# Kernel tuning notes

Hardware: AMD Instinct MI355X
Metric: run time of the kernel (lower is better)

Reference implementation:

```python
import jax, jax.numpy as jnp
import numpy as np

NV, T, CIN, CV, P, NB, H, W, G, SL = 50000, 16, 8, 64, 8, 120000, 512, 512, 16, 4
EPS = 1e-5


def mish(x):
    return x * jnp.tanh(jax.nn.softplus(x))


def bn(x, gamma, beta, axes):
    # BatchNorm in training mode: biased batch stats over `axes`.
    m = x.mean(axes, keepdims=True)
    v = x.var(axes, keepdims=True)
    return (x - m) * jax.lax.rsqrt(v + EPS) * gamma + beta


def fe3(x, Wt, g, b):
    # FELayer on 3D input [N, L, Cin]: Linear -> BN over channel -> Mish
    y = jnp.einsum('nlc,oc->nlo', x, Wt)
    return mish(bn(y, g, b, (0, 1)))


def vfe(x, Wt, g, b):
    # VFELayer: FELayer -> max over points -> broadcast-concat
    p = fe3(x, Wt, g, b)  # [N, T, C/2]
    a = p.max(axis=1, keepdims=True)
    return jnp.concatenate([p, jnp.broadcast_to(a, p.shape)], axis=2)


def setup_inputs() -> dict:
    key = jax.random.key(0)
    ks = jax.random.split(key, 32)
    wn = lambda k, s: jax.random.normal(k, s, jnp.float32) * 0.1
    gm = lambda k, s: 1.0 + jax.random.normal(k, s, jnp.float32) * 0.1
    bt = lambda k, s: jax.random.normal(k, s, jnp.float32) * 0.1
    inp = {}
    inp['voxels'] = jax.random.normal(ks[0], (NV, T, CIN), jnp.float32)
    inp['voxelmask'] = (jax.random.uniform(ks[1], (NV, T, 1)) > 0.2).astype(jnp.float32)
    inp['bevmask'] = (jax.random.uniform(ks[2], (NB, 1, P)) > 0.2).astype(jnp.float32)
    # params
    inp['W_vfe1'] = wn(ks[3], (8, CIN));   inp['g_vfe1'] = gm(ks[4], (8,));   inp['b_vfe1'] = bt(ks[5], (8,))
    inp['W_vfe2'] = wn(ks[6], (32, 16));   inp['g_vfe2'] = gm(ks[7], (32,));  inp['b_vfe2'] = bt(ks[8], (32,))
    inp['W_vfe3'] = wn(ks[9], (CV, CV));   inp['g_vfe3'] = gm(ks[10], (CV,)); inp['b_vfe3'] = bt(ks[11], (CV,))
    inp['W_vfe4'] = wn(ks[12], (CV, CV));  inp['g_vfe4'] = gm(ks[13], (CV,)); inp['b_vfe4'] = bt(ks[14], (CV,))
    inp['W_bfe1'] = wn(ks[15], (G, P, P)); inp['g_bfe1'] = gm(ks[16], (G, P)); inp['b_bfe1'] = bt(ks[17], (G, P))
    inp['W_bfe2'] = wn(ks[18], (G, 2, P)); inp['g_bfe2'] = gm(ks[19], (G, 2)); inp['b_bfe2'] = bt(ks[20], (G, 2))
    inp['W_bfe3'] = wn(ks[21], (128, 128)); inp['g_bfe3'] = gm(ks[22], (128,)); inp['b_bfe3'] = bt(ks[23], (128,))
    # int args
    inp['bevsidx'] = jax.random.randint(ks[24], (NB, P), 0, NV)
    flat = jax.random.permutation(ks[25], H * W)[:NB]  # unique scatter targets
    inp['bevcoors'] = jnp.stack([flat // W, flat % W], axis=1)
    return inp


def reference(voxels, voxelmask, bevmask,
              W_vfe1, g_vfe1, b_vfe1, W_vfe2, g_vfe2, b_vfe2,
              W_vfe3, g_vfe3, b_vfe3, W_vfe4, g_vfe4, b_vfe4,
              W_bfe1, g_bfe1, b_bfe1, W_bfe2, g_bfe2, b_bfe2,
              W_bfe3, g_bfe3, b_bfe3, bevsidx, bevcoors):
    x1 = vfe(voxels, W_vfe1, g_vfe1, b_vfe1)               # [NV, T, 16]
    x2 = vfe(x1, W_vfe2, g_vfe2, b_vfe2) * voxelmask       # [NV, T, 64]
    x3 = fe3(x2, W_vfe3, g_vfe3, b_vfe3)
    x4 = fe3(x3, W_vfe4, g_vfe4, b_vfe4) * voxelmask + x2
    voxelwise = x4.max(axis=1)                             # [NV, 64]

    bevs = voxelwise[bevsidx]                              # [NB, P, 64]
    # x0 = [NB, 64, P] -> 16 groups of 4 channel-slices -> [NB, G, SL, P]
    xg = bevs.transpose(0, 2, 1).reshape(bevs.shape[0], G, SL, P)
    h = jnp.einsum('ngcp,gqp->ngcq', xg, W_bfe1)           # [NB, G, SL, P]
    h = mish(bn(h, g_bfe1[:, None, :], b_bfe1[:, None, :], (0, 2)))
    h = h * bevmask[:, None]                               # [NB,1,1,P] broadcast
    h = jnp.einsum('ngcp,gqp->ngcq', h, W_bfe2)            # [NB, G, SL, 2]
    h = mish(bn(h, g_bfe2[:, None, :], b_bfe2[:, None, :], (0, 2)))
    # torch cat over dim=-1 across groups -> [NB, SL, G, 2] -> [NB, 128]
    x17 = h.transpose(0, 2, 1, 3).reshape(h.shape[0], 128)

    def bfe3(z):
        return mish(bn(z @ W_bfe3.T, g_bfe3, b_bfe3, (0,)))

    x18 = bfe3(x17)
    x19 = bfe3(x18) + x17                                  # NOTE: original reuses bfe3 (bfe4 unused)

    bevmap = jnp.zeros((H, W, 128), voxels.dtype)
    bevmap = bevmap.at[bevcoors[:, 0], bevcoors[:, 1]].set(x19)
    return bevmap.transpose(2, 1, 0)                       # [128, W, H]
```

## Files before the change

kernel.cpp:

```cpp
#include <hip/hip_runtime.h>
#include <math.h>

#define NV_   50000
#define T16_  16
#define NVT_  800000
#define NB_   120000
#define G_    16
#define P_    8
#define H_    512
#define W_    512

#define OF_Y34    0ul
#define OF_Y2     51200000ul
#define OF_Y1     76800000ul
#define OF_VW     83200000ul
#define OF_INV    86400000ul
#define OF_PRE17  0ul
#define OF_X17    16000000ul
#define OF_Y1819  32000000ul
#define STATS_BYTE 346648576ul

#define D_ST1 0
#define D_ST2 16
#define D_ST3 80
#define D_ST4 208
#define D_SB1 336
#define D_SB2 592
#define D_S18 656
#define D_S19 912
#define D_TOTAL 1168

#define LB_HEAVY __launch_bounds__(256, 2)
#define LB_LIGHT __launch_bounds__(256, 4)

__device__ __forceinline__ float mishf(float x) {
  float e = __expf(x);
  float u = 1.0f + e;
  return x - 2.0f * x / (u * u + 1.0f);
}

template <int N>
__device__ __forceinline__ void wave_red_sum(float* v) {
#pragma unroll
  for (int d = 1; d < 64; d <<= 1) {
#pragma unroll
    for (int i = 0; i < N; i++) v[i] += __shfl_xor(v[i], d, 64);
  }
}

__global__ void LB_LIGHT k_inv(const int* __restrict__ coors, int* __restrict__ inv) {
  int n = blockIdx.x * 256 + threadIdx.x;
  if (n < NB_) {
    int h = coors[2 * n], w = coors[2 * n + 1];
    inv[h * W_ + w] = n;
  }
}

__global__ void LB_LIGHT k1(const float* __restrict__ vox, const float* __restrict__ W1,
                   float* __restrict__ y1, double* __restrict__ st) {
  __shared__ float wl[64];
  __shared__ float lst[16];
  int t = threadIdx.x;
  if (t < 64) wl[t] = W1[t];
  if (t < 16) lst[t] = 0.f;
  __syncthreads();
  size_t s = (size_t)blockIdx.x * 256 + t;
  const float4* vp = (const float4*)(vox + s * 8);
  float4 a0 = vp[0], a1 = vp[1];
  float x[8] = {a0.x, a0.y, a0.z, a0.w, a1.x, a1.y, a1.z, a1.w};
  float y[8];
#pragma unroll
  for (int o = 0; o < 8; o++) {
    float a = 0.f;
#pragma unroll
    for (int c = 0; c < 8; c++) a += x[c] * wl[o * 8 + c];
    y[o] = a;
  }
  float4* yp = (float4*)(y1 + s * 8);
  yp[0] = make_float4(y[0], y[1], y[2], y[3]);
  yp[1] = make_float4(y[4], y[5], y[6], y[7]);
  float v[16];
#pragma unroll
  for (int i = 0; i < 8; i++) { v[i] = y[i]; v[8 + i] = y[i] * y[i]; }
  wave_red_sum<16>(v);
  if ((t & 63) == 0) {
#pragma unroll
    for (int i = 0; i < 16; i++) atomicAdd(&lst[i], v[i]);
  }
  __syncthreads();
  if (t < 16) atomicAdd(&st[t], (double)lst[t]);
}

__global__ void LB_HEAVY k2(const float* __restrict__ y1, const double* __restrict__ st1,
                   const float* __restrict__ g1, const float* __restrict__ b1,
                   const float* __restrict__ W2, float* __restrict__ y2,
                   double* __restrict__ st2) {
  __shared__ float wl[512];
  __shared__ float ab[8][2];
  __shared__ float lst[64];
  int t = threadIdx.x;
  wl[t] = W2[t];
  wl[256 + t] = W2[256 + t];
  if (t < 8) {
    double m = st1[t] / (double)NVT_;
    double var = st1[8 + t] / (double)NVT_ - m * m;
    if (var < 0) var = 0;
    float A = (float)((double)g1[t] / sqrt(var + 1e-5));
    ab[t][0] = A; ab[t][1] = b1[t] - (float)m * A;
  }
  if (t < 64) lst[t] = 0.f;
  __syncthreads();
  size_t s = (size_t)blockIdx.x * 256 + t;
  const float4* yp = (const float4*)(y1 + s * 8);
  float4 f0 = yp[0], f1 = yp[1];
  float in[8] = {f0.x, f0.y, f0.z, f0.w, f1.x, f1.y, f1.z, f1.w};
  float xr[16];
#pragma unroll
  for (int c = 0; c < 8; c++) xr[c] = mishf(in[c] * ab[c][0] + ab[c][1]);
#pragma unroll
  for (int c = 0; c < 8; c++) xr[8 + c] = xr[c];
#pragma unroll
  for (int d = 1; d < 16; d <<= 1) {
#pragma unroll
    for (int c = 0; c < 8; c++)
      xr[8 + c] = fmaxf(xr[8 + c], __shfl_xor(xr[8 + c], d, 64));
  }
  float yo[32];
#pragma unroll
  for (int o = 0; o < 32; o++) {
    float a = 0.f;
    const float4* wp = (const float4*)(wl + o * 16);
#pragma unroll
    for (int c4 = 0; c4 < 4; c4++) {
      float4 w4 = wp[c4];
      a += xr[c4 * 4 + 0] * w4.x + xr[c4 * 4 + 1] * w4.y +
           xr[c4 * 4 + 2] * w4.z + xr[c4 * 4 + 3] * w4.w;
    }
    yo[o] = a;
  }
  float4* op = (float4*)(y2 + s * 32);
#pragma unroll
  for (int j = 0; j < 8; j++)
    op[j] = make_float4(yo[j * 4], yo[j * 4 + 1], yo[j * 4 + 2], yo[j * 4 + 3]);
#pragma unroll
  for (int ch = 0; ch < 4; ch++) {
    float v[16];
#pragma unroll
    for (int i = 0; i < 8; i++) {
      v[i] = yo[ch * 8 + i]; v[8 + i] = v[i] * v[i];
    }
    wave_red_sum<16>(v);
    if ((t & 63) == 0) {
#pragma unroll
      for (int i = 0; i < 8; i++) {
        atomicAdd(&lst[ch * 8 + i], v[i]);
        atomicAdd(&lst[32 + ch * 8 + i], v[8 + i]);
      }
    }
  }
  __syncthreads();
  if (t < 64) atomicAdd(&st2[t], (double)lst[t]);
}

__global__ void LB_HEAVY k3(const float* __restrict__ y2, const double* __restrict__ st2,
                   const float* __restrict__ g2, const float* __restrict__ b2,
                   const float* __restrict__ vmask, const float* __restrict__ W3,
                   float* __restrict__ y3, double* __restrict__ st3) {
  __shared__ float ab[32][2];
  __shared__ float lst[128];
  int t = threadIdx.x;
  if (t < 32) {
    double m = st2[t] / (double)NVT_;
    double var = st2[32 + t] / (double)NVT_ - m * m;
    if (var < 0) var = 0;
    float A = (float)((double)g2[t] / sqrt(var + 1e-5));
    ab[t][0] = A; ab[t][1] = b2[t] - (float)m * A;
  }
  if (t < 128) lst[t] = 0.f;
  __syncthreads();
  size_t s = (size_t)blockIdx.x * 256 + t;
  float xr[64];
  const float4* yp = (const float4*)(y2 + s * 32);
#pragma unroll
  for (int j = 0; j < 8; j++) {
    float4 f = yp[j];
    xr[j * 4 + 0] = mishf(f.x * ab[j * 4 + 0][0] + ab[j * 4 + 0][1]);
    xr[j * 4 + 1] = mishf(f.y * ab[j * 4 + 1][0] + ab[j * 4 + 1][1]);
    xr[j * 4 + 2] = mishf(f.z * ab[j * 4 + 2][0] + ab[j * 4 + 2][1]);
    xr[j * 4 + 3] = mishf(f.w * ab[j * 4 + 3][0] + ab[j * 4 + 3][1]);
  }
#pragma unroll
  for (int c = 0; c < 32; c++) xr[32 + c] = xr[c];
#pragma unroll
  for (int d = 1; d < 16; d <<= 1) {
#pragma unroll
    for (int c = 0; c < 32; c++)
      xr[32 + c] = fmaxf(xr[32 + c], __shfl_xor(xr[32 + c], d, 64));
  }
  float m = vmask[s];
#pragma unroll
  for (int c = 0; c < 64; c++) xr[c] *= m;
#pragma unroll
  for (int oc = 0; oc < 4; oc++) {
    float yo[16];
#pragma unroll
    for (int o = 0; o < 16; o++) {
      float a = 0.f;
      const float4* wp = (const float4*)(W3 + (oc * 16 + o) * 64);
#pragma unroll
      for (int c4 = 0; c4 < 16; c4++) {
        float4 w4 = wp[c4];
        a += xr[c4 * 4 + 0] * w4.x + xr[c4 * 4 + 1] * w4.y +
             xr[c4 * 4 + 2] * w4.z + xr[c4 * 4 + 3] * w4.w;
      }
      yo[o] = a;
    }
    float4* op = (float4*)(y3 + s * 64 + oc * 16);
#pragma unroll
    for (int j = 0; j < 4; j++)
      op[j] = make_float4(yo[j * 4], yo[j * 4 + 1], yo[j * 4 + 2], yo[j * 4 + 3]);
    float v[32];
#pragma unroll
    for (int i = 0; i < 16; i++) { v[i] = yo[i]; v[16 + i] = yo[i] * yo[i]; }
    wave_red_sum<32>(v);
    if ((t & 63) == 0) {
#pragma unroll
      for (int i = 0; i < 16; i++) {
        atomicAdd(&lst[oc * 16 + i], v[i]);
        atomicAdd(&lst[64 + oc * 16 + i], v[16 + i]);
      }
    }
  }
  __syncthreads();
  if (t < 128) atomicAdd(&st3[t], (double)lst[t]);
}

__global__ void LB_HEAVY k4(float* y34, const double* __restrict__ st3,
                   const float* __restrict__ g3, const float* __restrict__ b3,
                   const float* __restrict__ W4, double* __restrict__ st4) {
  __shared__ float ab[64][2];
  __shared__ float lst[128];
  int t = threadIdx.x;
  if (t < 64) {
    double m = st3[t] / (double)NVT_;
    double var = st3[64 + t] / (double)NVT_ - m * m;
    if (var < 0) var = 0;
    float A = (float)((double)g3[t] / sqrt(var + 1e-5));
    ab[t][0] = A; ab[t][1] = b3[t] - (float)m * A;
  }
  if (t < 128) lst[t] = 0.f;
  __syncthreads();
  size_t s = (size_t)blockIdx.x * 256 + t;
  float xr[64];
  const float4* yp = (const float4*)(y34 + s * 64);
#pragma unroll
  for (int j = 0; j < 16; j++) {
    float4 f = yp[j];
    xr[j * 4 + 0] = mishf(f.x * ab[j * 4 + 0][0] + ab[j * 4 + 0][1]);
    xr[j * 4 + 1] = mishf(f.y * ab[j * 4 + 1][0] + ab[j * 4 + 1][1]);
    xr[j * 4 + 2] = mishf(f.z * ab[j * 4 + 2][0] + ab[j * 4 + 2][1]);
    xr[j * 4 + 3] = mishf(f.w * ab[j * 4 + 3][0] + ab[j * 4 + 3][1]);
  }
#pragma unroll
  for (int oc = 0; oc < 4; oc++) {
    float yo[16];
#pragma unroll
    for (int o = 0; o < 16; o++) {
      float a = 0.f;
      const float4* wp = (const float4*)(W4 + (oc * 16 + o) * 64);
#pragma unroll
      for (int c4 = 0; c4 < 16; c4++) {
        float4 w4 = wp[c4];
        a += xr[c4 * 4 + 0] * w4.x + xr[c4 * 4 + 1] * w4.y +
             xr[c4 * 4 + 2] * w4.z + xr[c4 * 4 + 3] * w4.w;
      }
      yo[o] = a;
    }
    float4* op = (float4*)(y34 + s * 64 + oc * 16);
#pragma unroll
    for (int j = 0; j < 4; j++)
      op[j] = make_float4(yo[j * 4], yo[j * 4 + 1], yo[j * 4 + 2], yo[j * 4 + 3]);
    float v[32];
#pragma unroll
    for (int i = 0; i < 16; i++) { v[i] = yo[i]; v[16 + i] = yo[i] * yo[i]; }
    wave_red_sum<32>(v);
    if ((t & 63) == 0) {
#pragma unroll
      for (int i = 0; i < 16; i++) {
        atomicAdd(&lst[oc * 16 + i], v[i]);
        atomicAdd(&lst[64 + oc * 16 + i], v[16 + i]);
      }
    }
  }
  __syncthreads();
  if (t < 128) atomicAdd(&st4[t], (double)lst[t]);
}

__global__ void LB_HEAVY k5(const float* __restrict__ y34, const double* __restrict__ st4,
                   const float* __restrict__ g4, const float* __restrict__ b4,
                   const float* __restrict__ y2, const double* __restrict__ st2,
                   const float* __restrict__ g2, const float* __restrict__ b2,
                   const float* __restrict__ vmask, float* __restrict__ vw) {
  __shared__ float ab4[64][2];
  __shared__ float ab2[32][2];
  int t = threadIdx.x;
  if (t < 64) {
    double m = st4[t] / (double)NVT_;
    double var = st4[64 + t] / (double)NVT_ - m * m;
    if (var < 0) var = 0;
    float A = (float)((double)g4[t] / sqrt(var + 1e-5));
    ab4[t][0] = A; ab4[t][1] = b4[t] - (float)m * A;
  } else if (t >= 128 && t < 160) {
    int c = t - 128;
    double m = st2[c] / (double)NVT_;
    double var = st2[32 + c] / (double)NVT_ - m * m;
    if (var < 0) var = 0;
    float A = (float)((double)g2[c] / sqrt(var + 1e-5));
    ab2[c][0] = A; ab2[c][1] = b2[c] - (float)m * A;
  }
  __syncthreads();
  size_t s = (size_t)blockIdx.x * 256 + t;
  int v = (int)(s >> 4), ti = t & 15;
  float msk = vmask[s];
  float xr[64];
  const float4* y2p = (const float4*)(y2 + s * 32);
#pragma unroll
  for (int j = 0; j < 8; j++) {
    float4 f = y2p[j];
    xr[j * 4 + 0] = mishf(f.x * ab2[j * 4 + 0][0] + ab2[j * 4 + 0][1]);
    xr[j * 4 + 1] = mishf(f.y * ab2[j * 4 + 1][0] + ab2[j * 4 + 1][1]);
    xr[j * 4 + 2] = mishf(f.z * ab2[j * 4 + 2][0] + ab2[j * 4 + 2][1]);
    xr[j * 4 + 3] = mishf(f.w * ab2[j * 4 + 3][0] + ab2[j * 4 + 3][1]);
  }
#pragma unroll
  for (int c = 0; c < 32; c++) xr[32 + c] = xr[c];
#pragma unroll
  for (int d = 1; d < 16; d <<= 1) {
#pragma unroll
    for (int c = 0; c < 32; c++)
      xr[32 + c] = fmaxf(xr[32 + c], __shfl_xor(xr[32 + c], d, 64));
  }
#pragma unroll
  for (int c = 0; c < 64; c++) xr[c] *= msk;
  const float4* yp = (const float4*)(y34 + s * 64);
#pragma unroll
  for (int j = 0; j < 16; j++) {
    float4 f = yp[j];
    xr[j * 4 + 0] += mishf(f.x * ab4[j * 4 + 0][0] + ab4[j * 4 + 0][1]) * msk;
    xr[j * 4 + 1] += mishf(f.y * ab4[j * 4 + 1][0] + ab4[j * 4 + 1][1]) * msk;
    xr[j * 4 + 2] += mishf(f.z * ab4[j * 4 + 2][0] + ab4[j * 4 + 2][1]) * msk;
    xr[j * 4 + 3] += mishf(f.w * ab4[j * 4 + 3][0] + ab4[j * 4 + 3][1]) * msk;
  }
#pragma unroll
  for (int d = 1; d < 16; d <<= 1) {
#pragma unroll
    for (int c = 0; c < 64; c++)
      xr[c] = fmaxf(xr[c], __shfl_xor(xr[c], d, 64));
  }
  *(float4*)(vw + (size_t)v * 64 + ti * 4) =
      make_float4(xr[ti * 4], xr[ti * 4 + 1], xr[ti * 4 + 2], xr[ti * 4 + 3]);
}

__global__ void LB_HEAVY k6(const float* __restrict__ vw, const int* __restrict__ idx,
                   const float* __restrict__ Wb1, double* __restrict__ sb1) {
  __shared__ float wl[1024];
  __shared__ float lst[256];
  int t = threadIdx.x;
  for (int i = t; i < 1024; i += 256) {
    int g = i >> 6, qp = i & 63;
    wl[qp * 16 + g] = Wb1[i];
  }
  lst[t] = 0.f;
  __syncthreads();
  int g = t & 15, nl = t >> 4;
  float ss[8] = {0, 0, 0, 0, 0, 0, 0, 0}, sq[8] = {0, 0, 0, 0, 0, 0, 0, 0};
  for (int it = 0; it < 16; ++it) {
    int n = blockIdx.x * 256 + it * 16 + nl;
    if (n < NB_) {
      int id[8];
#pragma unroll
      for (int p = 0; p < 8; p++) id[p] = idx[n * 8 + p];
      float xg[4][8];
#pragma unroll
      for (int p = 0; p < 8; p++) {
        float4 f = *(const float4*)(vw + (size_t)id[p] * 64 + g * 4);
        xg[0][p] = f.x; xg[1][p] = f.y; xg[2][p] = f.z; xg[3][p] = f.w;
      }
#pragma unroll
      for (int q = 0; q < 8; q++) {
        float wq[8];
#pragma unroll
        for (int p = 0; p < 8; p++) wq[p] = wl[(q * 8 + p) * 16 + g];
#pragma unroll
        for (int c = 0; c < 4; c++) {
          float a = 0.f;
#pragma unroll
          for (int p = 0; p < 8; p++) a += xg[c][p] * wq[p];
          ss[q] += a; sq[q] += a * a;
        }
      }
    }
  }
#pragma unroll
  for (int d = 16; d < 64; d <<= 1) {
#pragma unroll
    for (int q = 0; q < 8; q++) {
      ss[q] += __shfl_xor(ss[q], d, 64);
      sq[q] += __shfl_xor(sq[q], d, 64);
    }
  }
  if ((t & 48) == 0) {
#pragma unroll
    for (int q = 0; q < 8; q++) {
      atomicAdd(&lst[g * 8 + q], ss[q]);
      atomicAdd(&lst[128 + g * 8 + q], sq[q]);
    }
  }
  __syncthreads();
  atomicAdd(&sb1[t], (double)lst[t]);
}

__global__ void LB_HEAVY k7(const float* __restrict__ vw, const int* __restrict__ idx,
                   const float* __restrict__ Wb1, const double* __restrict__ sb1,
                   const float* __restrict__ gb1, const float* __restrict__ bb1,
                   const float* __restrict__ bmask, const float* __restrict__ Wb2,
                   float* __restrict__ pre17, double* __restrict__ sb2) {
  __shared__ float wl[1024];
  __shared__ float w2l[256];
  __shared__ float ab[128][2];
  __shared__ float lst[64];
  int t = threadIdx.x;
  for (int i = t; i < 1024; i += 256) {
    int g = i >> 6, qp = i & 63;
    wl[qp * 16 + g] = Wb1[i];
  }
  {
    int g = t >> 4, qq = t & 15;
    w2l[qq * 16 + g] = Wb2[t];
  }
  if (t < 128) {
    double m = sb1[t] / 480000.0;
    double var = sb1[128 + t] / 480000.0 - m * m;
    if (var < 0) var = 0;
    float A = (float)((double)gb1[t] / sqrt(var + 1e-5));
    ab[t][0] = A; ab[t][1] = bb1[t] - (float)m * A;
  }
  if (t < 64) lst[t] = 0.f;
  __syncthreads();
  int g = t & 15, nl = t >> 4;
  float s2[2] = {0, 0}, q2s[2] = {0, 0};
  for (int it = 0; it < 16; ++it) {
    int n = blockIdx.x * 256 + it * 16 + nl;
    if (n < NB_) {
      int id[8];
      float bmv[8];
#pragma unroll
      for (int p = 0; p < 8; p++) { id[p] = idx[n * 8 + p]; bmv[p] = bmask[n * 8 + p]; }
      float xg[4][8];
#pragma unroll
      for (int p = 0; p < 8; p++) {
        float4 f = *(const float4*)(vw + (size_t)id[p] * 64 + g * 4);
        xg[0][p] = f.x; xg[1][p] = f.y; xg[2][p] = f.z; xg[3][p] = f.w;
      }
      float th[4][8];
#pragma unroll
      for (int q = 0; q < 8; q++) {
        float wq[8];
#pragma unroll
        for (int p = 0; p < 8; p++) wq[p] = wl[(q * 8 + p) * 16 + g];
        float A = ab[g * 8 + q][0], B = ab[g * 8 + q][1];
#pragma unroll
        for (int c = 0; c < 4; c++) {
          float a = 0.f;
#pragma unroll
          for (int p = 0; p < 8; p++) a += xg[c][p] * wq[p];
          th[c][q] = mishf(a * A + B) * bmv[q];
        }
      }
#pragma unroll
      for (int c = 0; c < 4; c++) {
        float v0 = 0.f, v1 = 0.f;
#pragma unroll
        for (int q = 0; q < 8; q++) {
          v0 += th[c][q] * w2l[q * 16 + g];
          v1 += th[c][q] * w2l[(8 + q) * 16 + g];
        }
        *(float2*)(pre17 + (size_t)n * 128 + c * 32 + g * 2) = make_float2(v0, v1);
        s2[0] += v0; q2s[0] += v0 * v0;
        s2[1] += v1; q2s[1] += v1 * v1;
      }
    }
  }
#pragma unroll
  for (int d = 16; d < 64; d <<= 1) {
#pragma unroll
    for (int j = 0; j < 2; j++) {
      s2[j] += __shfl_xor(s2[j], d, 64);
      q2s[j] += __shfl_xor(q2s[j], d, 64);
    }
  }
  if ((t & 48) == 0) {
#pragma unroll
    for (int j = 0; j < 2; j++) {
      atomicAdd(&lst[g * 2 + j], s2[j]);
      atomicAdd(&lst[32 + g * 2 + j], q2s[j]);
    }
  }
  __syncthreads();
  if (t < 64) atomicAdd(&sb2[t], (double)lst[t]);
}

template <int MODE>
__global__ void LB_HEAVY kgemm(const float* xin, const double* __restrict__ stin,
                      const float* __restrict__ gam, const float* __restrict__ bet,
                      const float* __restrict__ Wt, float* xact_out,
                      float* yout, double* __restrict__ stout) {
  __shared__ float xs[32 * 129];
  __shared__ float wsh[128 * 33];
  __shared__ float ab[128][2];
  __shared__ float lst[256];
  int t = threadIdx.x;
  const int nch = (MODE == 0) ? 32 : 128;
  const double den = (MODE == 0) ? 480000.0 : 120000.0;
  if (t < nch) {
    double m = stin[t] / den;
    double var = stin[nch + t] / den - m * m;
    if (var < 0) var = 0;
    float A = (float)((double)gam[t] / sqrt(var + 1e-5));
    ab[t][0] = A; ab[t][1] = bet[t] - (float)m * A;
  }
  lst[t] = 0.f;
  __syncthreads();
  int s0 = blockIdx.x * 128;
  int oc = t & 7, sc = t >> 3;
  int cl = t & 31, sl8 = t >> 5;
  float acc[64];
#pragma unroll
  for (int i = 0; i < 64; i++) acc[i] = 0.f;
  for (int cb = 0; cb < 128; cb += 32) {
#pragma unroll
    for (int r = 0; r < 16; r++) {
      int slocal = r * 8 + sl8;
      int sg = s0 + slocal;
      float v = 0.f;
      if (sg < NB_) {
        float h = xin[(size_t)sg * 128 + cb + cl];
        if (MODE == 0) {
          v = mishf(h * ab[cl][0] + ab[cl][1]);
          xact_out[(size_t)sg * 128 + cb + cl] = v;
        } else {
          v = mishf(h * ab[cb + cl][0] + ab[cb + cl][1]);
        }
      }
      xs[cl * 129 + slocal] = v;
    }
#pragma unroll
    for (int r = 0; r < 16; r++) {
      int o = r * 8 + sl8;
      wsh[o * 33 + cl] = Wt[o * 128 + cb + cl];
    }
    __syncthreads();
#pragma unroll 4
    for (int c = 0; c < 32; c++) {
      float xv[4];
#pragma unroll
      for (int i = 0; i < 4; i++) xv[i] = xs[c * 129 + sc * 4 + i];
#pragma unroll
      for (int k = 0; k < 16; k++) {
        float wv = wsh[(k * 8 + oc) * 33 + c];
#pragma unroll
        for (int i = 0; i < 4; i++) acc[k * 4 + i] += wv * xv[i];
      }
    }
    __syncthreads();
  }
  float ssum[16], ssq[16];
#pragma unroll
  for (int k = 0; k < 16; k++) { ssum[k] = 0.f; ssq[k] = 0.f; }
#pragma unroll
  for (int i = 0; i < 4; i++) {
    int sg = s0 + sc * 4 + i;
    if (sg < NB_) {
#pragma unroll
      for (int k = 0; k < 16; k++) {
        float v = acc[k * 4 + i];
        yout[(size_t)sg * 128 + k * 8 + oc] = v;
        ssum[k] += v; ssq[k] += v * v;
      }
    }
  }
#pragma unroll
  for (int d = 8; d < 64; d <<= 1) {
#pragma unroll
    for (int k = 0; k < 16; k++) {
      ssum[k] += __shfl_xor(ssum[k], d, 64);
      ssq[k] += __shfl_xor(ssq[k], d, 64);
    }
  }
  if ((t & 63) < 8) {
#pragma unroll
    for (int k = 0; k < 16; k++) {
      atomicAdd(&lst[k * 8 + oc], ssum[k]);
      atomicAdd(&lst[128 + k * 8 + oc], ssq[k]);
    }
  }
  __syncthreads();
  atomicAdd(&stout[t], (double)lst[t]);
}

__global__ void LB_LIGHT k10(const float* __restrict__ y19, const float* __restrict__ x17,
                    const double* __restrict__ s19, const float* __restrict__ g3,
                    const float* __restrict__ b3, const int* __restrict__ inv,
                    float* __restrict__ out) {
  __shared__ float buf[256 * 32];
  __shared__ float ab[32][2];
  int t = threadIdx.x;
  int w = blockIdx.x, hh = blockIdx.y, ch = blockIdx.z;
  if (t < 32) {
    int c = ch * 32 + t;
    double m = s19[c] / 120000.0;
    double var = s19[128 + c] / 120000.0 - m * m;
    if (var < 0) var = 0;
    float A = (float)((double)g3[c] / sqrt(var + 1e-5));
    ab[t][0] = A; ab[t][1] = b3[c] - (float)m * A;
  }
  __syncthreads();
  int lane = t & 31, rg = t >> 5;
#pragma unroll 4
  for (int r = 0; r < 32; r++) {
    int h_l = r * 8 + rg;
    int h = hh * 256 + h_l;
    int n = inv[h * W_ + w];
    float v = 0.f;
    if (n >= 0) {
      float y = y19[(size_t)n * 128 + ch * 32 + lane];
      v = mishf(y * ab[lane][0] + ab[lane][1]) +
          x17[(size_t)n * 128 + ch * 32 + lane];
    }
    buf[h_l * 32 + (lane ^ (h_l & 31))] = v;
  }
  __syncthreads();
#pragma unroll 4
  for (int c_l = 0; c_l < 32; c_l++) {
    out[(size_t)(ch * 32 + c_l) * (W_ * H_) + (size_t)w * H_ + hh * 256 + t] =
        buf[t * 32 + (c_l ^ (t & 31))];
  }
}

extern "C" void kernel_launch(void* const* d_in, const int* in_sizes, int n_in,
                              void* d_out, int out_size, void* d_ws, size_t ws_size,
                              hipStream_t stream) {
  const float* voxels = (const float*)d_in[0];
  const float* vmask = (const float*)d_in[1];
  const float* bmask = (const float*)d_in[2];
  const float* W1 = (const float*)d_in[3];
  const float* g1 = (const float*)d_in[4];
  const float* b1 = (const float*)d_in[5];
  const float* W2 = (const float*)d_in[6];
  const float* g2 = (const float*)d_in[7];
  const float* b2 = (const float*)d_in[8];
  const float* W3 = (const float*)d_in[9];
  const float* g3 = (const float*)d_in[10];
  const float* b3 = (const float*)d_in[11];
  const float* W4 = (const float*)d_in[12];
  const float* g4 = (const float*)d_in[13];
  const float* b4 = (const float*)d_in[14];
  const float* Wb1 = (const float*)d_in[15];
  const float* gb1 = (const float*)d_in[16];
  const float* bb1 = (const float*)d_in[17];
  const float* Wb2 = (const float*)d_in[18];
  const float* gb2 = (const float*)d_in[19];
  const float* bb2 = (const float*)d_in[20];
  const float* Wb3 = (const float*)d_in[21];
  const float* gb3 = (const float*)d_in[22];
  const float* bb3 = (const float*)d_in[23];
  const int* bevsidx = (const int*)d_in[24];
  const int* bevcoors = (const int*)d_in[25];

  float* ws = (float*)d_ws;
  float* y1 = ws + OF_Y1;
  float* y2 = ws + OF_Y2;
  float* y34 = ws + OF_Y34;
  float* vw = ws + OF_VW;
  float* pre17 = ws + OF_PRE17;
  float* x17 = ws + OF_X17;
  float* y1819 = ws + OF_Y1819;
  int* inv = (int*)(ws + OF_INV);
  double* stats = (double*)((char*)d_ws + STATS_BYTE);

  hipMemsetAsync(stats, 0, D_TOTAL * sizeof(double), stream);
  hipMemsetAsync(inv, 0xFF, (size_t)(H_ * W_) * sizeof(int), stream);

  k_inv<<<469, 256, 0, stream>>>(bevcoors, inv);
  k1<<<3125, 256, 0, stream>>>(voxels, W1, y1, stats + D_ST1);
  k2<<<3125, 256, 0, stream>>>(y1, stats + D_ST1, g1, b1, W2, y2, stats + D_ST2);
  k3<<<3125, 256, 0, stream>>>(y2, stats + D_ST2, g2, b2, vmask, W3, y34,
                               stats + D_ST3);
  k4<<<3125, 256, 0, stream>>>(y34, stats + D_ST3, g3, b3, W4, stats + D_ST4);
  k5<<<3125, 256, 0, stream>>>(y34, stats + D_ST4, g4, b4, y2, stats + D_ST2,
                               g2, b2, vmask, vw);
  k6<<<469, 256, 0, stream>>>(vw, bevsidx, Wb1, stats + D_SB1);
  k7<<<469, 256, 0, stream>>>(vw, bevsidx, Wb1, stats + D_SB1, gb1, bb1, bmask,
                              Wb2, pre17, stats + D_SB2);
  kgemm<0><<<938, 256, 0, stream>>>(pre17, stats + D_SB2, gb2, bb2, Wb3, x17,
                                    y1819, stats + D_S18);
  kgemm<1><<<938, 256, 0, stream>>>(y1819, stats + D_S18, gb3, bb3, Wb3, nullptr,
                                    y1819, stats + D_S19);
  dim3 g10(512, 2, 4);
  k10<<<g10, 256, 0, stream>>>(y1819, x17, stats + D_S19, gb3, bb3, inv,
                               (float*)d_out);
}
```

Measured before the change: 1.707 ms.

## Restructure VFE3/VFE4 GEMMs: weights in registers, rows staged through shared memory

k3 and k4 previously gave each thread one point row. Each thread held 64 activations and re-read all 64x64 weights from global/cache, then did heavy wave shuffles for the stats. Now each thread owns one output channel with its weight row in registers. Blocks loop over 16-row chunks staged in shared memory (mish, max-over-points and mask done cooperatively), and per-channel sums are accumulated in registers so the shuffle reductions go away. This trades register pressure and weight reloads for more barriers per chunk and a fixed 2500x20x16 tiling of the 800000 rows.

```diff
diff --git a/kernel.cpp b/kernel.cpp
--- a/kernel.cpp
+++ b/kernel.cpp
@@ -33,6 +33,9 @@
 #define LB_HEAVY __launch_bounds__(256, 2)
 #define LB_LIGHT __launch_bounds__(256, 4)
 
+#define GEMM_BLOCKS 2500
+#define GEMM_CHUNKS 20
+
 __device__ __forceinline__ float mishf(float x) {
   float e = __expf(x);
   float u = 1.0f + e;
@@ -162,13 +165,19 @@
   if (t < 64) atomicAdd(&st2[t], (double)lst[t]);
 }
 
-__global__ void LB_HEAVY k3(const float* __restrict__ y2, const double* __restrict__ st2,
-                   const float* __restrict__ g2, const float* __restrict__ b2,
-                   const float* __restrict__ vmask, const float* __restrict__ W3,
-                   float* __restrict__ y3, double* __restrict__ st3) {
+__global__ void __launch_bounds__(256, 4)
+k3(const float* __restrict__ y2, const double* __restrict__ st2,
+   const float* __restrict__ g2, const float* __restrict__ b2,
+   const float* __restrict__ vmask, const float* __restrict__ W3,
+   float* __restrict__ y3, double* __restrict__ st3) {
   __shared__ float ab[32][2];
+  __shared__ float x2s[16][32];
+  __shared__ float xmax[32];
+  __shared__ float msk[16];
+  __shared__ float xs[16][64];
   __shared__ float lst[128];
   int t = threadIdx.x;
+  int o = t & 63, wv = t >> 6;
   if (t < 32) {
     double m = st2[t] / (double)NVT_;
     double var = st2[32 + t] / (double)NVT_ - m * m;
@@ -177,70 +186,76 @@
     ab[t][0] = A; ab[t][1] = b2[t] - (float)m * A;
   }
   if (t < 128) lst[t] = 0.f;
-  __syncthreads();
-  size_t s = (size_t)blockIdx.x * 256 + t;
-  float xr[64];
-  const float4* yp = (const float4*)(y2 + s * 32);
-#pragma unroll
-  for (int j = 0; j < 8; j++) {
-    float4 f = yp[j];
-    xr[j * 4 + 0] = mishf(f.x * ab[j * 4 + 0][0] + ab[j * 4 + 0][1]);
-    xr[j * 4 + 1] = mishf(f.y * ab[j * 4 + 1][0] + ab[j * 4 + 1][1]);
-    xr[j * 4 + 2] = mishf(f.z * ab[j * 4 + 2][0] + ab[j * 4 + 2][1]);
-    xr[j * 4 + 3] = mishf(f.w * ab[j * 4 + 3][0] + ab[j * 4 + 3][1]);
-  }
-#pragma unroll
-  for (int c = 0; c < 32; c++) xr[32 + c] = xr[c];
-#pragma unroll
-  for (int d = 1; d < 16; d <<= 1) {
-#pragma unroll
-    for (int c = 0; c < 32; c++)
-      xr[32 + c] = fmaxf(xr[32 + c], __shfl_xor(xr[32 + c], d, 64));
-  }
-  float m = vmask[s];
-#pragma unroll
-  for (int c = 0; c < 64; c++) xr[c] *= m;
-#pragma unroll
-  for (int oc = 0; oc < 4; oc++) {
-    float yo[16];
-#pragma unroll
-    for (int o = 0; o < 16; o++) {
+  float4 w[16];
+#pragma unroll
+  for (int i = 0; i < 16; i++) w[i] = *(const float4*)(W3 + o * 64 + i * 4);
+  __syncthreads();
+  float ssum = 0.f, ssq = 0.f;
+  for (int ch = 0; ch < GEMM_CHUNKS; ++ch) {
+    size_t base = ((size_t)blockIdx.x * GEMM_CHUNKS + ch) * 16;
+    {
+      float2 f = *(const float2*)(y2 + base * 32 + t * 2);
+      int c0 = (t * 2) & 31;
+      x2s[t >> 4][(t & 15) * 2 + 0] = mishf(f.x * ab[c0][0] + ab[c0][1]);
+      x2s[t >> 4][(t & 15) * 2 + 1] = mishf(f.y * ab[c0 + 1][0] + ab[c0 + 1][1]);
+    }
+    if (t < 16) msk[t] = vmask[base + t];
+    __syncthreads();
+    if (t < 32) {
+      float m = x2s[0][t];
+#pragma unroll
+      for (int r = 1; r < 16; r++) m = fmaxf(m, x2s[r][t]);
+      xmax[t] = m;
+    }
+    __syncthreads();
+    {
+      int row = t >> 4, c0 = (t & 15) * 4;
+      float mk = msk[row];
+      if (c0 < 32) {
+#pragma unroll
+        for (int j = 0; j < 4; j++) xs[row][c0 + j] = x2s[row][c0 + j] * mk;
+      } else {
+#pragma unroll
+        for (int j = 0; j < 4; j++) xs[row][c0 + j] = xmax[c0 - 32 + j] * mk;
+      }
+    }
+    __syncthreads();
+    float acc[4];
+#pragma unroll
+    for (int r = 0; r < 4; r++) {
+      int row = wv * 4 + r;
+      const float4* xp = (const float4*)xs[row];
       float a = 0.f;
-      const float4* wp = (const float4*)(W3 + (oc * 16 + o) * 64);
-#pragma unroll
-      for (int c4 = 0; c4 < 16; c4++) {
-        float4 w4 = wp[c4];
-        a += xr[c4 * 4 + 0] * w4.x + xr[c4 * 4 + 1] * w4.y +
-             xr[c4 * 4 + 2] * w4.z + xr[c4 * 4 + 3] * w4.w;
-      }
-      yo[o] = a;
-    }
-    float4* op = (float4*)(y3 + s * 64 + oc * 16);
-#pragma unroll
-    for (int j = 0; j < 4; j++)
-      op[j] = make_float4(yo[j * 4], yo[j * 4 + 1], yo[j * 4 + 2], yo[j * 4 + 3]);
-    float v[32];
-#pragma unroll
-    for (int i = 0; i < 16; i++) { v[i] = yo[i]; v[16 + i] = yo[i] * yo[i]; }
-    wave_red_sum<32>(v);
-    if ((t & 63) == 0) {
 #pragma unroll
       for (int i = 0; i < 16; i++) {
-        atomicAdd(&lst[oc * 16 + i], v[i]);
-        atomicAdd(&lst[64 + oc * 16 + i], v[16 + i]);
-      }
-    }
-  }
+        float4 x4 = xp[i];
+        a += x4.x * w[i].x + x4.y * w[i].y + x4.z * w[i].z + x4.w * w[i].w;
+      }
+      acc[r] = a;
+    }
+#pragma unroll
+    for (int r = 0; r < 4; r++) {
+      int row = wv * 4 + r;
+      y3[(base + row) * 64 + o] = acc[r];
+      ssum += acc[r]; ssq += acc[r] * acc[r];
+    }
+    __syncthreads();
+  }
+  atomicAdd(&lst[o], ssum);
+  atomicAdd(&lst[64 + o], ssq);
   __syncthreads();
   if (t < 128) atomicAdd(&st3[t], (double)lst[t]);
 }
 
-__global__ void LB_HEAVY k4(float* y34, const double* __restrict__ st3,
-                   const float* __restrict__ g3, const float* __restrict__ b3,
-                   const float* __restrict__ W4, double* __restrict__ st4) {
+__global__ void __launch_bounds__(256, 4)
+k4(float* y34, const double* __restrict__ st3,
+   const float* __restrict__ g3, const float* __restrict__ b3,
+   const float* __restrict__ W4, double* __restrict__ st4) {
   __shared__ float ab[64][2];
+  __shared__ float xs[16][64];
   __shared__ float lst[128];
   int t = threadIdx.x;
+  int o = t & 63, wv = t >> 6;
   if (t < 64) {
     double m = st3[t] / (double)NVT_;
     double var = st3[64 + t] / (double)NVT_ - m * m;
@@ -249,49 +264,47 @@
     ab[t][0] = A; ab[t][1] = b3[t] - (float)m * A;
   }
   if (t < 128) lst[t] = 0.f;
-  __syncthreads();
-  size_t s = (size_t)blockIdx.x * 256 + t;
-  float xr[64];
-  const float4* yp = (const float4*)(y34 + s * 64);
-#pragma unroll
-  for (int j = 0; j < 16; j++) {
-    float4 f = yp[j];
-    xr[j * 4 + 0] = mishf(f.x * ab[j * 4 + 0][0] + ab[j * 4 + 0][1]);
-    xr[j * 4 + 1] = mishf(f.y * ab[j * 4 + 1][0] + ab[j * 4 + 1][1]);
-    xr[j * 4 + 2] = mishf(f.z * ab[j * 4 + 2][0] + ab[j * 4 + 2][1]);
-    xr[j * 4 + 3] = mishf(f.w * ab[j * 4 + 3][0] + ab[j * 4 + 3][1]);
-  }
-#pragma unroll
-  for (int oc = 0; oc < 4; oc++) {
-    float yo[16];
-#pragma unroll
-    for (int o = 0; o < 16; o++) {
+  float4 w[16];
+#pragma unroll
+  for (int i = 0; i < 16; i++) w[i] = *(const float4*)(W4 + o * 64 + i * 4);
+  __syncthreads();
+  float ssum = 0.f, ssq = 0.f;
+  for (int ch = 0; ch < GEMM_CHUNKS; ++ch) {
+    size_t base = ((size_t)blockIdx.x * GEMM_CHUNKS + ch) * 16;
+    {
+      float4 f = *(const float4*)(y34 + base * 64 + t * 4);
+      int c0 = (t * 4) & 63;
+      float4 v;
+      v.x = mishf(f.x * ab[c0 + 0][0] + ab[c0 + 0][1]);
+      v.y = mishf(f.y * ab[c0 + 1][0] + ab[c0 + 1][1]);
+      v.z = mishf(f.z * ab[c0 + 2][0] + ab[c0 + 2][1]);
+      v.w = mishf(f.w * ab[c0 + 3][0] + ab[c0 + 3][1]);
+      *(float4*)(&xs[t >> 4][(t & 15) * 4]) = v;
+    }
+    __syncthreads();
+    float acc[4];
+#pragma unroll
+    for (int r = 0; r < 4; r++) {
+      int row = wv * 4 + r;
+      const float4* xp = (const float4*)xs[row];
       float a = 0.f;
-      const float4* wp = (const float4*)(W4 + (oc * 16 + o) * 64);
-#pragma unroll
-      for (int c4 = 0; c4 < 16; c4++) {
-        float4 w4 = wp[c4];
-        a += xr[c4 * 4 + 0] * w4.x + xr[c4 * 4 + 1] * w4.y +
-             xr[c4 * 4 + 2] * w4.z + xr[c4 * 4 + 3] * w4.w;
-      }
-      yo[o] = a;
-    }
-    float4* op = (float4*)(y34 + s * 64 + oc * 16);
-#pragma unroll
-    for (int j = 0; j < 4; j++)
-      op[j] = make_float4(yo[j * 4], yo[j * 4 + 1], yo[j * 4 + 2], yo[j * 4 + 3]);
-    float v[32];
-#pragma unroll
-    for (int i = 0; i < 16; i++) { v[i] = yo[i]; v[16 + i] = yo[i] * yo[i]; }
-    wave_red_sum<32>(v);
-    if ((t & 63) == 0) {
 #pragma unroll
       for (int i = 0; i < 16; i++) {
-        atomicAdd(&lst[oc * 16 + i], v[i]);
-        atomicAdd(&lst[64 + oc * 16 + i], v[16 + i]);
-      }
-    }
-  }
+        float4 x4 = xp[i];
+        a += x4.x * w[i].x + x4.y * w[i].y + x4.z * w[i].z + x4.w * w[i].w;
+      }
+      acc[r] = a;
+    }
+#pragma unroll
+    for (int r = 0; r < 4; r++) {
+      int row = wv * 4 + r;
+      y34[(base + row) * 64 + o] = acc[r];
+      ssum += acc[r]; ssq += acc[r] * acc[r];
+    }
+    __syncthreads();
+  }
+  atomicAdd(&lst[o], ssum);
+  atomicAdd(&lst[64 + o], ssq);
   __syncthreads();
   if (t < 128) atomicAdd(&st4[t], (double)lst[t]);
 }
@@ -694,9 +707,10 @@
   k_inv<<<469, 256, 0, stream>>>(bevcoors, inv);
   k1<<<3125, 256, 0, stream>>>(voxels, W1, y1, stats + D_ST1);
   k2<<<3125, 256, 0, stream>>>(y1, stats + D_ST1, g1, b1, W2, y2, stats + D_ST2);
-  k3<<<3125, 256, 0, stream>>>(y2, stats + D_ST2, g2, b2, vmask, W3, y34,
-                               stats + D_ST3);
-  k4<<<3125, 256, 0, stream>>>(y34, stats + D_ST3, g3, b3, W4, stats + D_ST4);
+  k3<<<GEMM_BLOCKS, 256, 0, stream>>>(y2, stats + D_ST2, g2, b2, vmask, W3, y34,
+                                      stats + D_ST3);
+  k4<<<GEMM_BLOCKS, 256, 0, stream>>>(y34, stats + D_ST3, g3, b3, W4,
+                                      stats + D_ST4);
   k5<<<3125, 256, 0, stream>>>(y34, stats + D_ST4, g4, b4, y2, stats + D_ST2,
                                g2, b2, vmask, vw);
   k6<<<469, 256, 0, stream>>>(vw, bevsidx, Wb1, stats + D_SB1);
```

New measurement: 1.444 ms. 1.18x faster.
